# Kernel optimization log

Hardware: AMD Instinct MI355X
Metric: run time of the kernel (lower is better)

Reference implementation:

```python
import jax, jax.numpy as jnp
import numpy as np

B, S, D, DS = 32, 1024, 256, 64
M = 3  # modalities: audio, visual, lexical


def setup_inputs() -> dict:
    key = jax.random.key(0)
    ks = jax.random.split(key, 16)
    w = 0.05
    return {
        "x_audio": jax.random.normal(ks[0], (B, S, D), jnp.float32),
        "x_visual": jax.random.normal(ks[1], (B, S, D), jnp.float32),
        "x_lexical": jax.random.normal(ks[2], (B, S, D), jnp.float32),
        "XW": jax.random.normal(ks[3], (M, DS, D), jnp.float32) * w,
        "Xb": jax.random.normal(ks[4], (M, DS), jnp.float32) * w,
        "HW": jax.random.normal(ks[5], (M, DS, DS), jnp.float32) * w,
        "Hb": jax.random.normal(ks[6], (M, DS), jnp.float32) * w,
        "OW": jax.random.normal(ks[7], (M, D, DS), jnp.float32) * w,
        "Ob": jax.random.normal(ks[8], (M, D), jnp.float32) * w,
        "CW": jax.random.normal(ks[9], (M, M, DS, DS), jnp.float32) * w,
        "W1": jax.random.normal(ks[10], (DS, M * DS), jnp.float32) * w,
        "b1": jax.random.normal(ks[11], (DS,), jnp.float32) * w,
        "W2": jax.random.normal(ks[12], (M * M, DS), jnp.float32) * w,
        "b2": jax.random.normal(ks[13], (M * M,), jnp.float32) * w,
        "ln_g": jnp.ones((M, D), jnp.float32),
        "ln_b": jnp.zeros((M, D), jnp.float32),
    }


def _layernorm(x, g, b, eps=1e-5):
    mu = jnp.mean(x, axis=-1, keepdims=True)
    var = jnp.mean(jnp.square(x - mu), axis=-1, keepdims=True)
    return (x - mu) * jax.lax.rsqrt(var + eps) * g + b


def reference(x_audio, x_visual, x_lexical, XW, Xb, HW, Hb, OW, Ob, CW,
              W1, b1, W2, b2, ln_g, ln_b):
    x = jnp.stack([x_audio, x_visual, x_lexical], axis=0)  # [M,B,S,D]
    xs = x.transpose(2, 0, 1, 3)                            # [S,M,B,D]
    mask = 1.0 - jnp.eye(M, dtype=x.dtype)                  # src != tgt

    def step(h, x_t):
        # h: [M,B,DS], x_t: [M,B,D]
        hc = h.transpose(1, 0, 2).reshape(h.shape[1], M * DS)      # [B, M*DS]
        raw = jnp.tanh(hc @ W1.T + b1) @ W2.T + b2                 # [B, M*M]
        attn = jax.nn.softmax(raw.reshape(-1, M, M), axis=-1)      # [B, tgt, src]
        hproj = jnp.einsum('tsde,sbe->tsbd', CW, h)                # [tgt,src,B,DS]
        coupling = jnp.einsum('bts,ts,tsbd->tbd', attn, mask, hproj)
        su = (jnp.einsum('mde,mbe->mbd', HW, h) + Hb[:, None, :]
              + jnp.einsum('mdk,mbk->mbd', XW, x_t) + Xb[:, None, :]
              + coupling)
        h_new = jax.nn.silu(su)                                    # [M,B,DS]
        y = jnp.einsum('mkd,mbd->mbk', OW, h_new) + Ob[:, None, :]  # [M,B,D]
        return h_new, y

    h0 = jnp.zeros((M, x.shape[1], DS), x.dtype)
    _, ys = jax.lax.scan(step, h0, xs)          # [S,M,B,D]
    out = ys.transpose(1, 2, 0, 3) + x          # residual, [M,B,S,D]
    out = _layernorm(out, ln_g[:, None, None, :], ln_b[:, None, None, :])
    return (out[0], out[1], out[2])
```

## Files before the change

### kernel.cpp

```cpp
#include <hip/hip_runtime.h>
#include <math.h>

#define B_  32
#define S_  1024
#define D_  256
#define DS_ 64
#define M_  3
#define MD_ 192

#define BAR_LGKM() asm volatile("s_waitcnt lgkmcnt(0)\n\ts_barrier" ::: "memory")

__device__ __forceinline__ float rl_f32(float v, int lane) {
    return __uint_as_float(__builtin_amdgcn_readlane(__float_as_uint(v), lane));
}

#define L2E_ 1.4426950408889634f
__device__ __forceinline__ float fast_exp(float x) { return exp2f(x * L2E_); }
__device__ __forceinline__ float fast_tanh(float x) {
    float t = exp2f(x * (2.0f * L2E_));
    return 1.0f - 2.0f * __builtin_amdgcn_rcpf(t + 1.0f);
}

typedef float v4f __attribute__((ext_vector_type(4)));

#define ALD4(dst, p, off) \
    asm volatile("global_load_dwordx4 %0, %1, off offset:" #off \
                 : "=v"(dst) : "v"(p))

#define DECL_W16A(baseptr) \
    v4f W00, W01, W02, W03, W04, W05, W06, W07, \
        W08, W09, W10, W11, W12, W13, W14, W15; \
    { const float* _wp = (baseptr); \
      ALD4(W00, _wp, 0);   ALD4(W01, _wp, 16);  ALD4(W02, _wp, 32);  ALD4(W03, _wp, 48);  \
      ALD4(W04, _wp, 64);  ALD4(W05, _wp, 80);  ALD4(W06, _wp, 96);  ALD4(W07, _wp, 112); \
      ALD4(W08, _wp, 128); ALD4(W09, _wp, 144); ALD4(W10, _wp, 160); ALD4(W11, _wp, 176); \
      ALD4(W12, _wp, 192); ALD4(W13, _wp, 208); ALD4(W14, _wp, 224); ALD4(W15, _wp, 240); \
      asm volatile("s_waitcnt vmcnt(0)" ::: "memory"); }

#define DOT4_RL(Wv, k0) \
    a0 = fmaf(Wv.x, rl_f32(hreg, (k0) + 0), a0); \
    a1 = fmaf(Wv.y, rl_f32(hreg, (k0) + 1), a1); \
    a2 = fmaf(Wv.z, rl_f32(hreg, (k0) + 2), a2); \
    a3 = fmaf(Wv.w, rl_f32(hreg, (k0) + 3), a3);
#define DOT64_RL() \
    DOT4_RL(W00, 0)  DOT4_RL(W01, 4)  DOT4_RL(W02, 8)  DOT4_RL(W03, 12) \
    DOT4_RL(W04, 16) DOT4_RL(W05, 20) DOT4_RL(W06, 24) DOT4_RL(W07, 28) \
    DOT4_RL(W08, 32) DOT4_RL(W09, 36) DOT4_RL(W10, 40) DOT4_RL(W11, 44) \
    DOT4_RL(W12, 48) DOT4_RL(W13, 52) DOT4_RL(W14, 56) DOT4_RL(W15, 60)

#define DOT4_V(Wv, hv) \
    a0 = fmaf(Wv.x, (hv).x, a0); \
    a1 = fmaf(Wv.y, (hv).y, a1); \
    a2 = fmaf(Wv.z, (hv).z, a2); \
    a3 = fmaf(Wv.w, (hv).w, a3);
#define DOT64_V(h4) \
    DOT4_V(W00, (h4)[0])  DOT4_V(W01, (h4)[1])  DOT4_V(W02, (h4)[2])  DOT4_V(W03, (h4)[3])  \
    DOT4_V(W04, (h4)[4])  DOT4_V(W05, (h4)[5])  DOT4_V(W06, (h4)[6])  DOT4_V(W07, (h4)[7])  \
    DOT4_V(W08, (h4)[8])  DOT4_V(W09, (h4)[9])  DOT4_V(W10, (h4)[10]) DOT4_V(W11, (h4)[11]) \
    DOT4_V(W12, (h4)[12]) DOT4_V(W13, (h4)[13]) DOT4_V(W14, (h4)[14]) DOT4_V(W15, (h4)[15])

#define DPP_RED3(A, Bv, C) asm volatile( \
    "v_add_f32 %0, %0, %0 row_shr:1 bound_ctrl:0\n\t" \
    "v_add_f32 %1, %1, %1 row_shr:1 bound_ctrl:0\n\t" \
    "v_add_f32 %2, %2, %2 row_shr:1 bound_ctrl:0\n\t" \
    "v_add_f32 %0, %0, %0 row_shr:2 bound_ctrl:0\n\t" \
    "v_add_f32 %1, %1, %1 row_shr:2 bound_ctrl:0\n\t" \
    "v_add_f32 %2, %2, %2 row_shr:2 bound_ctrl:0\n\t" \
    "v_add_f32 %0, %0, %0 row_shr:4 bound_ctrl:0\n\t" \
    "v_add_f32 %1, %1, %1 row_shr:4 bound_ctrl:0\n\t" \
    "v_add_f32 %2, %2, %2 row_shr:4 bound_ctrl:0\n\t" \
    "v_add_f32 %0, %0, %0 row_shr:8 bound_ctrl:0\n\t" \
    "v_add_f32 %1, %1, %1 row_shr:8 bound_ctrl:0\n\t" \
    "v_add_f32 %2, %2, %2 row_shr:8 bound_ctrl:0\n\t" \
    "v_add_f32 %0, %0, %0 row_bcast:15 row_mask:0xa\n\t" \
    "v_add_f32 %1, %1, %1 row_bcast:15 row_mask:0xa\n\t" \
    "v_add_f32 %2, %2, %2 row_bcast:15 row_mask:0xa\n\t" \
    "v_add_f32 %0, %0, %0 row_bcast:31 row_mask:0xc\n\t" \
    "v_add_f32 %1, %1, %1 row_bcast:31 row_mask:0xc\n\t" \
    "v_add_f32 %2, %2, %2 row_bcast:31 row_mask:0xc" \
    : "+v"(A), "+v"(Bv), "+v"(C))

#define DPP_RED4(A, Bv, C, Dv) asm volatile( \
    "v_add_f32 %0, %0, %0 row_shr:1 bound_ctrl:0\n\t" \
    "v_add_f32 %1, %1, %1 row_shr:1 bound_ctrl:0\n\t" \
    "v_add_f32 %2, %2, %2 row_shr:1 bound_ctrl:0\n\t" \
    "v_add_f32 %3, %3, %3 row_shr:1 bound_ctrl:0\n\t" \
    "v_add_f32 %0, %0, %0 row_shr:2 bound_ctrl:0\n\t" \
    "v_add_f32 %1, %1, %1 row_shr:2 bound_ctrl:0\n\t" \
    "v_add_f32 %2, %2, %2 row_shr:2 bound_ctrl:0\n\t" \
    "v_add_f32 %3, %3, %3 row_shr:2 bound_ctrl:0\n\t" \
    "v_add_f32 %0, %0, %0 row_shr:4 bound_ctrl:0\n\t" \
    "v_add_f32 %1, %1, %1 row_shr:4 bound_ctrl:0\n\t" \
    "v_add_f32 %2, %2, %2 row_shr:4 bound_ctrl:0\n\t" \
    "v_add_f32 %3, %3, %3 row_shr:4 bound_ctrl:0\n\t" \
    "v_add_f32 %0, %0, %0 row_shr:8 bound_ctrl:0\n\t" \
    "v_add_f32 %1, %1, %1 row_shr:8 bound_ctrl:0\n\t" \
    "v_add_f32 %2, %2, %2 row_shr:8 bound_ctrl:0\n\t" \
    "v_add_f32 %3, %3, %3 row_shr:8 bound_ctrl:0\n\t" \
    "v_add_f32 %0, %0, %0 row_bcast:15 row_mask:0xa\n\t" \
    "v_add_f32 %1, %1, %1 row_bcast:15 row_mask:0xa\n\t" \
    "v_add_f32 %2, %2, %2 row_bcast:15 row_mask:0xa\n\t" \
    "v_add_f32 %3, %3, %3 row_bcast:15 row_mask:0xa\n\t" \
    "v_add_f32 %0, %0, %0 row_bcast:31 row_mask:0xc\n\t" \
    "v_add_f32 %1, %1, %1 row_bcast:31 row_mask:0xc\n\t" \
    "v_add_f32 %2, %2, %2 row_bcast:31 row_mask:0xc\n\t" \
    "v_add_f32 %3, %3, %3 row_bcast:31 row_mask:0xc" \
    : "+v"(A), "+v"(Bv), "+v"(C), "+v"(Dv))

__global__ __launch_bounds__(256, 2)
void k1_xproj(const float* __restrict__ xa, const float* __restrict__ xv,
              const float* __restrict__ xl, const float* __restrict__ XW,
              const float* __restrict__ Xb, float* __restrict__ xp)
{
    const int m  = blockIdx.z;
    const int b  = blockIdx.y;
    const int t0 = blockIdx.x * 128;
    const float* __restrict__ xm = (m == 0) ? xa : ((m == 1) ? xv : xl);
    const int tid = threadIdx.x;
    const int q = tid >> 6;
    const int d = tid & 63;

    __shared__ __align__(16) float xs[4][256];
    __shared__ float part[4][4][64];

    DECL_W16A(XW + ((m * 64 + d) * 256 + q * 64));
    const float xbv = Xb[m * 64 + d];

    for (int g = 0; g < 32; ++g) {
        const int tb = t0 + g * 4;
        {
            const float* src = xm + ((size_t)b * S_ + tb) * D_;
            xs[0][tid] = src[0 * 256 + tid];
            xs[1][tid] = src[1 * 256 + tid];
            xs[2][tid] = src[2 * 256 + tid];
            xs[3][tid] = src[3 * 256 + tid];
        }
        __syncthreads();
        #pragma unroll
        for (int tt = 0; tt < 4; ++tt) {
            const v4f* xq = reinterpret_cast<const v4f*>(&xs[tt][q * 64]);
            float a0 = 0.f, a1 = 0.f, a2 = 0.f, a3 = 0.f;
            DOT64_V(xq);
            part[tt][q][d] = (a0 + a1) + (a2 + a3);
        }
        __syncthreads();
        {
            const int tt = q;
            float ssum = part[tt][0][d] + part[tt][1][d] + part[tt][2][d] + part[tt][3][d] + xbv;
            xp[((size_t)b * S_ + tb + tt) * MD_ + m * 64 + d] = ssum;
        }
    }
}

__global__ __launch_bounds__(768, 1)
void k2_recur(const float* __restrict__ xp, float* __restrict__ hbuf,
              const float* __restrict__ HW, const float* __restrict__ Hb,
              const float* __restrict__ CW, const float* __restrict__ W1,
              const float* __restrict__ b1, const float* __restrict__ W2,
              const float* __restrict__ b2)
{
    const int b    = blockIdx.x;
    const int tid  = threadIdx.x;
    const int w    = tid >> 6;
    const int lane = tid & 63;

    const bool is_gate = (w >= 9);
    const int  m = is_gate ? (w - 9) : (w / 3);
    const int  s = is_gate ? (w - 9) : (w % 3);

    __shared__ __align__(16) float hds[2][MD_];
    __shared__ float parts[12][64];

    if (tid < MD_) hds[0][tid] = 0.f;

    const float* base;
    if (!is_gate) base = (s == m) ? (HW + (m * 64 + lane) * 64)
                                  : (CW + (((m * 3 + s) * 64) + lane) * 64);
    else          base = W1 + lane * MD_ + m * 64;
    DECL_W16A(base);

    float hbv = 0.f, b1v = 0.f;
    float w2r0 = 0.f, w2r1 = 0.f, w2r2 = 0.f, b2v0 = 0.f, b2v1 = 0.f, b2v2 = 0.f;
    float xnext = 0.f;
    if (is_gate) {
        hbv  = Hb[m * 64 + lane];
        b1v  = b1[lane];
        w2r0 = W2[(m * 3 + 0) * 64 + lane];
        w2r1 = W2[(m * 3 + 1) * 64 + lane];
        w2r2 = W2[(m * 3 + 2) * 64 + lane];
        b2v0 = b2[m * 3 + 0]; b2v1 = b2[m * 3 + 1]; b2v2 = b2[m * 3 + 2];
        xnext = xp[((size_t)b * S_) * MD_ + m * 64 + lane];
    }
    const int s1 = (m + 1) % 3, s2 = (m + 2) % 3;
    float hist0 = 0.f, hist1 = 0.f, hist2 = 0.f, hist3 = 0.f;

    __syncthreads();

    for (int t = 0; t < S_; ++t) {
        const int cur = t & 1, nxt = cur ^ 1;

        const float xv = xnext;
        if (is_gate && (t + 1 < S_))
            xnext = xp[((size_t)b * S_ + t + 1) * MD_ + m * 64 + lane];

        float hreg = hds[cur][s * 64 + lane];
        float a0 = 0.f, a1 = 0.f, a2 = 0.f, a3 = 0.f;
        DOT64_RL();
        parts[w][lane] = (a0 + a1) + (a2 + a3);
        BAR_LGKM();

        if (is_gate) {
            float pm  = parts[m * 3 + m][lane];
            float pc1 = parts[m * 3 + s1][lane];
            float pc2 = parts[m * 3 + s2][lane];
            float g0  = parts[9][lane];
            float g1  = parts[10][lane];
            float g2  = parts[11][lane];

            float z = fast_tanh(b1v + g0 + g1 + g2);
            float p0 = w2r0 * z, p1 = w2r1 * z, p2 = w2r2 * z;
            DPP_RED3(p0, p1, p2);
            float r0 = b2v0 + rl_f32(p0, 63);
            float r1 = b2v1 + rl_f32(p1, 63);
            float r2 = b2v2 + rl_f32(p2, 63);
            float mx  = fmaxf(r0, fmaxf(r1, r2));
            float e0  = fast_exp(r0 - mx);
            float e1  = fast_exp(r1 - mx);
            float e2  = fast_exp(r2 - mx);
            float inv = __builtin_amdgcn_rcpf(e0 + e1 + e2);
            float a1v = ((s1 == 1) ? e1 : (s1 == 2) ? e2 : e0) * inv;
            float a2v = ((s2 == 1) ? e1 : (s2 == 2) ? e2 : e0) * inv;

            float suv = xv + hbv + pm + a1v * pc1 + a2v * pc2;
            float hn  = suv * __builtin_amdgcn_rcpf(1.f + fast_exp(-suv));
            hds[nxt][m * 64 + lane] = hn;

            if      ((t & 3) == 0) hist0 = hn;
            else if ((t & 3) == 1) hist1 = hn;
            else if ((t & 3) == 2) hist2 = hn;
            else {
                hist3 = hn;
                float* dst = hbuf + ((size_t)b * S_ + (t - 3)) * MD_ + m * 64 + lane;
                dst[0 * MD_] = hist0; dst[1 * MD_] = hist1;
                dst[2 * MD_] = hist2; dst[3 * MD_] = hist3;
            }
        }
        BAR_LGKM();
    }
}

__global__ __launch_bounds__(256, 2)
void k3_out(const float* __restrict__ xa, const float* __restrict__ xv,
            const float* __restrict__ xl, const float* __restrict__ hbuf,
            const float* __restrict__ OW, const float* __restrict__ Ob,
            const float* __restrict__ lng, const float* __restrict__ lnb,
            float* __restrict__ out)
{
    const int m  = blockIdx.z;
    const int b  = blockIdx.y;
    const int t0 = blockIdx.x * 128;
    const float* __restrict__ xm = (m == 0) ? xa : ((m == 1) ? xv : xl);
    const int k    = threadIdx.x;
    const int wv   = k >> 6;
    const int lane = k & 63;

    __shared__ __align__(16) float hs[4 * 64];
    __shared__ float psum[16], qsum[16];

    DECL_W16A(OW + (m * D_ + k) * DS_);
    const float obv = Ob[m * D_ + k];
    const float gv  = lng[m * D_ + k];
    const float bv  = lnb[m * D_ + k];

    for (int gg = 0; gg < 32; ++gg) {
        const int tb = t0 + gg * 4;
        hs[k] = hbuf[((size_t)b * S_ + tb + (k >> 6)) * MD_ + m * 64 + (k & 63)];
        __syncthreads();

        float v0, v1, v2, v3;
        {
            const v4f* h4 = reinterpret_cast<const v4f*>(&hs[0]);
            float a0 = 0.f, a1 = 0.f, a2 = 0.f, a3 = 0.f;
            DOT64_V(h4);
            v0 = obv + (a0 + a1) + (a2 + a3) + xm[((size_t)b * S_ + tb + 0) * D_ + k];
        }
        {
            const v4f* h4 = reinterpret_cast<const v4f*>(&hs[64]);
            float a0 = 0.f, a1 = 0.f, a2 = 0.f, a3 = 0.f;
            DOT64_V(h4);
            v1 = obv + (a0 + a1) + (a2 + a3) + xm[((size_t)b * S_ + tb + 1) * D_ + k];
        }
        {
            const v4f* h4 = reinterpret_cast<const v4f*>(&hs[128]);
            float a0 = 0.f, a1 = 0.f, a2 = 0.f, a3 = 0.f;
            DOT64_V(h4);
            v2 = obv + (a0 + a1) + (a2 + a3) + xm[((size_t)b * S_ + tb + 2) * D_ + k];
        }
        {
            const v4f* h4 = reinterpret_cast<const v4f*>(&hs[192]);
            float a0 = 0.f, a1 = 0.f, a2 = 0.f, a3 = 0.f;
            DOT64_V(h4);
            v3 = obv + (a0 + a1) + (a2 + a3) + xm[((size_t)b * S_ + tb + 3) * D_ + k];
        }

        float s0 = v0, s1v = v1, s2v = v2, s3 = v3;
        float q0 = v0 * v0, q1 = v1 * v1, q2 = v2 * v2, q3 = v3 * v3;
        DPP_RED4(s0, s1v, s2v, s3);
        DPP_RED4(q0, q1, q2, q3);
        if (lane == 63) {
            psum[wv * 4 + 0] = s0;  psum[wv * 4 + 1] = s1v;
            psum[wv * 4 + 2] = s2v; psum[wv * 4 + 3] = s3;
            qsum[wv * 4 + 0] = q0;  qsum[wv * 4 + 1] = q1;
            qsum[wv * 4 + 2] = q2;  qsum[wv * 4 + 3] = q3;
        }
        __syncthreads();

        const size_t obase = (size_t)m * ((size_t)B_ * S_ * D_) + ((size_t)b * S_ + tb) * D_ + k;
        {
            float ss = psum[0] + psum[4] + psum[8] + psum[12];
            float qq = qsum[0] + qsum[4] + qsum[8] + qsum[12];
            float mu = ss * (1.f / 256.f);
            float var = qq * (1.f / 256.f) - mu * mu;
            float rs = rsqrtf(var + 1e-5f);
            out[obase + 0 * D_] = (v0 - mu) * rs * gv + bv;
        }
        {
            float ss = psum[1] + psum[5] + psum[9] + psum[13];
            float qq = qsum[1] + qsum[5] + qsum[9] + qsum[13];
            float mu = ss * (1.f / 256.f);
            float var = qq * (1.f / 256.f) - mu * mu;
            float rs = rsqrtf(var + 1e-5f);
            out[obase + 1 * D_] = (v1 - mu) * rs * gv + bv;
        }
        {
            float ss = psum[2] + psum[6] + psum[10] + psum[14];
            float qq = qsum[2] + qsum[6] + qsum[10] + qsum[14];
            float mu = ss * (1.f / 256.f);
            float var = qq * (1.f / 256.f) - mu * mu;
            float rs = rsqrtf(var + 1e-5f);
            out[obase + 2 * D_] = (v2 - mu) * rs * gv + bv;
        }
        {
            float ss = psum[3] + psum[7] + psum[11] + psum[15];
            float qq = qsum[3] + qsum[7] + qsum[11] + qsum[15];
            float mu = ss * (1.f / 256.f);
            float var = qq * (1.f / 256.f) - mu * mu;
            float rs = rsqrtf(var + 1e-5f);
            out[obase + 3 * D_] = (v3 - mu) * rs * gv + bv;
        }
    }
}

extern "C" void kernel_launch(void* const* d_in, const int* in_sizes, int n_in,
                              void* d_out, int out_size, void* d_ws, size_t ws_size,
                              hipStream_t stream)
{
    const float* xa  = (const float*)d_in[0];
    const float* xv  = (const float*)d_in[1];
    const float* xl  = (const float*)d_in[2];
    const float* XW  = (const float*)d_in[3];
    const float* Xb  = (const float*)d_in[4];
    const float* HW  = (const float*)d_in[5];
    const float* Hb  = (const float*)d_in[6];
    const float* OW  = (const float*)d_in[7];
    const float* Ob  = (const float*)d_in[8];
    const float* CW  = (const float*)d_in[9];
    const float* W1  = (const float*)d_in[10];
    const float* b1  = (const float*)d_in[11];
    const float* W2  = (const float*)d_in[12];
    const float* b2  = (const float*)d_in[13];
    const float* lng = (const float*)d_in[14];
    const float* lnb = (const float*)d_in[15];
    float* out = (float*)d_out;

    float* xp = (float*)d_ws;
    float* hb = xp + (size_t)B_ * S_ * MD_;

    k1_xproj<<<dim3(8, 32, 3), 256, 0, stream>>>(xa, xv, xl, XW, Xb, xp);
    k2_recur<<<dim3(32), 768, 0, stream>>>(xp, hb, HW, Hb, CW, W1, b1, W2, b2);
    k3_out  <<<dim3(8, 32, 3), 256, 0, stream>>>(xa, xv, xl, hb, OW, Ob, lng, lnb, out);
}
```

Measured before the change: 1.339 ms.

## Use packed v4f FMA dot products and LDS vector reads in recurrence

Replaces the scalar four-accumulator FMA dot products with vector-of-4 elementwise FMAs, which the compiler can lower to packed FP32 instructions (v_pk_fma_f32) on CDNA. In the recurrent kernel, the 64 readlane broadcasts of h are replaced by LDS vector reads of the state. The gate wave also reuses its own partial sum directly instead of re-reading it from LDS. Together these cut VALU and readlane instruction count on the serial critical path, at the cost of more LDS read traffic and a different summation order.

```diff
diff --git a/kernel.cpp b/kernel.cpp
--- a/kernel.cpp
+++ b/kernel.cpp
@@ -37,27 +37,26 @@
       ALD4(W12, _wp, 192); ALD4(W13, _wp, 208); ALD4(W14, _wp, 224); ALD4(W15, _wp, 240); \
       asm volatile("s_waitcnt vmcnt(0)" ::: "memory"); }
 
-#define DOT4_RL(Wv, k0) \
-    a0 = fmaf(Wv.x, rl_f32(hreg, (k0) + 0), a0); \
-    a1 = fmaf(Wv.y, rl_f32(hreg, (k0) + 1), a1); \
-    a2 = fmaf(Wv.z, rl_f32(hreg, (k0) + 2), a2); \
-    a3 = fmaf(Wv.w, rl_f32(hreg, (k0) + 3), a3);
-#define DOT64_RL() \
-    DOT4_RL(W00, 0)  DOT4_RL(W01, 4)  DOT4_RL(W02, 8)  DOT4_RL(W03, 12) \
-    DOT4_RL(W04, 16) DOT4_RL(W05, 20) DOT4_RL(W06, 24) DOT4_RL(W07, 28) \
-    DOT4_RL(W08, 32) DOT4_RL(W09, 36) DOT4_RL(W10, 40) DOT4_RL(W11, 44) \
-    DOT4_RL(W12, 48) DOT4_RL(W13, 52) DOT4_RL(W14, 56) DOT4_RL(W15, 60)
-
-#define DOT4_V(Wv, hv) \
-    a0 = fmaf(Wv.x, (hv).x, a0); \
-    a1 = fmaf(Wv.y, (hv).y, a1); \
-    a2 = fmaf(Wv.z, (hv).z, a2); \
-    a3 = fmaf(Wv.w, (hv).w, a3);
-#define DOT64_V(h4) \
-    DOT4_V(W00, (h4)[0])  DOT4_V(W01, (h4)[1])  DOT4_V(W02, (h4)[2])  DOT4_V(W03, (h4)[3])  \
-    DOT4_V(W04, (h4)[4])  DOT4_V(W05, (h4)[5])  DOT4_V(W06, (h4)[6])  DOT4_V(W07, (h4)[7])  \
-    DOT4_V(W08, (h4)[8])  DOT4_V(W09, (h4)[9])  DOT4_V(W10, (h4)[10]) DOT4_V(W11, (h4)[11]) \
-    DOT4_V(W12, (h4)[12]) DOT4_V(W13, (h4)[13]) DOT4_V(W14, (h4)[14]) DOT4_V(W15, (h4)[15])
+#define DOT64_PKV(h4, out) { \
+    v4f A0 = W00 * (h4)[0]; \
+    v4f A1 = W01 * (h4)[1]; \
+    v4f A2 = W02 * (h4)[2]; \
+    v4f A3 = W03 * (h4)[3]; \
+    A0 = __builtin_elementwise_fma(W04, (h4)[4],  A0); \
+    A1 = __builtin_elementwise_fma(W05, (h4)[5],  A1); \
+    A2 = __builtin_elementwise_fma(W06, (h4)[6],  A2); \
+    A3 = __builtin_elementwise_fma(W07, (h4)[7],  A3); \
+    A0 = __builtin_elementwise_fma(W08, (h4)[8],  A0); \
+    A1 = __builtin_elementwise_fma(W09, (h4)[9],  A1); \
+    A2 = __builtin_elementwise_fma(W10, (h4)[10], A2); \
+    A3 = __builtin_elementwise_fma(W11, (h4)[11], A3); \
+    A0 = __builtin_elementwise_fma(W12, (h4)[12], A0); \
+    A1 = __builtin_elementwise_fma(W13, (h4)[13], A1); \
+    A2 = __builtin_elementwise_fma(W14, (h4)[14], A2); \
+    A3 = __builtin_elementwise_fma(W15, (h4)[15], A3); \
+    v4f T = (A0 + A1) + (A2 + A3); \
+    out = (T.x + T.y) + (T.z + T.w); \
+}
 
 #define DPP_RED3(A, Bv, C) asm volatile( \
     "v_add_f32 %0, %0, %0 row_shr:1 bound_ctrl:0\n\t" \
@@ -120,7 +119,7 @@
     const int q = tid >> 6;
     const int d = tid & 63;
 
-    __shared__ __align__(16) float xs[4][256];
+    __shared__ __align__(16) float xs[1024];
     __shared__ float part[4][4][64];
 
     DECL_W16A(XW + ((m * 64 + d) * 256 + q * 64));
@@ -128,20 +127,15 @@
 
     for (int g = 0; g < 32; ++g) {
         const int tb = t0 + g * 4;
-        {
-            const float* src = xm + ((size_t)b * S_ + tb) * D_;
-            xs[0][tid] = src[0 * 256 + tid];
-            xs[1][tid] = src[1 * 256 + tid];
-            xs[2][tid] = src[2 * 256 + tid];
-            xs[3][tid] = src[3 * 256 + tid];
-        }
+        reinterpret_cast<v4f*>(xs)[tid] =
+            reinterpret_cast<const v4f*>(xm + ((size_t)b * S_ + tb) * D_)[tid];
         __syncthreads();
         #pragma unroll
         for (int tt = 0; tt < 4; ++tt) {
-            const v4f* xq = reinterpret_cast<const v4f*>(&xs[tt][q * 64]);
-            float a0 = 0.f, a1 = 0.f, a2 = 0.f, a3 = 0.f;
-            DOT64_V(xq);
-            part[tt][q][d] = (a0 + a1) + (a2 + a3);
+            const v4f* xq = reinterpret_cast<const v4f*>(&xs[tt * 256 + q * 64]);
+            float accv;
+            DOT64_PKV(xq, accv);
+            part[tt][q][d] = accv;
         }
         __syncthreads();
         {
@@ -203,21 +197,20 @@
         if (is_gate && (t + 1 < S_))
             xnext = xp[((size_t)b * S_ + t + 1) * MD_ + m * 64 + lane];
 
-        float hreg = hds[cur][s * 64 + lane];
-        float a0 = 0.f, a1 = 0.f, a2 = 0.f, a3 = 0.f;
-        DOT64_RL();
-        parts[w][lane] = (a0 + a1) + (a2 + a3);
+        const v4f* h4 = reinterpret_cast<const v4f*>(&hds[cur][s * 64]);
+        float accv;
+        DOT64_PKV(h4, accv);
+        parts[w][lane] = accv;
         BAR_LGKM();
 
         if (is_gate) {
             float pm  = parts[m * 3 + m][lane];
             float pc1 = parts[m * 3 + s1][lane];
             float pc2 = parts[m * 3 + s2][lane];
-            float g0  = parts[9][lane];
-            float g1  = parts[10][lane];
-            float g2  = parts[11][lane];
-
-            float z = fast_tanh(b1v + g0 + g1 + g2);
+            float go1 = parts[9 + s1][lane];
+            float go2 = parts[9 + s2][lane];
+
+            float z = fast_tanh(b1v + accv + go1 + go2);
             float p0 = w2r0 * z, p1 = w2r1 * z, p2 = w2r2 * z;
             DPP_RED3(p0, p1, p2);
             float r0 = b2v0 + rl_f32(p0, 63);
@@ -280,27 +273,23 @@
         float v0, v1, v2, v3;
         {
             const v4f* h4 = reinterpret_cast<const v4f*>(&hs[0]);
-            float a0 = 0.f, a1 = 0.f, a2 = 0.f, a3 = 0.f;
-            DOT64_V(h4);
-            v0 = obv + (a0 + a1) + (a2 + a3) + xm[((size_t)b * S_ + tb + 0) * D_ + k];
+            float accv; DOT64_PKV(h4, accv);
+            v0 = obv + accv + xm[((size_t)b * S_ + tb + 0) * D_ + k];
         }
         {
             const v4f* h4 = reinterpret_cast<const v4f*>(&hs[64]);
-            float a0 = 0.f, a1 = 0.f, a2 = 0.f, a3 = 0.f;
-            DOT64_V(h4);
-            v1 = obv + (a0 + a1) + (a2 + a3) + xm[((size_t)b * S_ + tb + 1) * D_ + k];
+            float accv; DOT64_PKV(h4, accv);
+            v1 = obv + accv + xm[((size_t)b * S_ + tb + 1) * D_ + k];
         }
         {
             const v4f* h4 = reinterpret_cast<const v4f*>(&hs[128]);
-            float a0 = 0.f, a1 = 0.f, a2 = 0.f, a3 = 0.f;
-            DOT64_V(h4);
-            v2 = obv + (a0 + a1) + (a2 + a3) + xm[((size_t)b * S_ + tb + 2) * D_ + k];
+            float accv; DOT64_PKV(h4, accv);
+            v2 = obv + accv + xm[((size_t)b * S_ + tb + 2) * D_ + k];
         }
         {
             const v4f* h4 = reinterpret_cast<const v4f*>(&hs[192]);
-            float a0 = 0.f, a1 = 0.f, a2 = 0.f, a3 = 0.f;
-            DOT64_V(h4);
-            v3 = obv + (a0 + a1) + (a2 + a3) + xm[((size_t)b * S_ + tb + 3) * D_ + k];
+            float accv; DOT64_PKV(h4, accv);
+            v3 = obv + accv + xm[((size_t)b * S_ + tb + 3) * D_ + k];
         }
 
         float s0 = v0, s1v = v1, s2v = v2, s3 = v3;
```

Result: faster. 1.239 ms (-7.5%).
